# Kernel optimization log

Hardware: AMD Instinct MI355X
Metric: run time of the kernel (lower is better)

The kernel has to match this reference:

```python
import jax, jax.numpy as jnp
import numpy as np

EPS = 1e-5  # torch LayerNorm default

def _layernorm(x, g, b):
    mu = jnp.mean(x, axis=-1, keepdims=True)
    var = jnp.mean(jnp.square(x - mu), axis=-1, keepdims=True)
    return (x - mu) * jax.lax.rsqrt(var + EPS) * g + b

def _gelu(x):
    return jax.nn.gelu(x, approximate=False)  # torch nn.GELU default is exact erf

def setup_inputs() -> dict:
    B, S, D, F = 2, 128, 64, 256
    key = jax.random.key(0)
    ks = jax.random.split(key, 8)
    def xavier(k, fan_in, fan_out, gain=1.0):
        lim = gain * np.sqrt(6.0 / (fan_in + fan_out))
        return jax.random.uniform(k, (fan_in, fan_out), jnp.float32, -lim, lim)
    return {
        "q": jax.random.normal(ks[0], (B, S, D), jnp.float32),
        # gauge generator MLP: Linear(2D, F) -> GELU -> Linear(F, D*D)
        "gw1": xavier(ks[1], 2 * D, F),
        "gb1": jnp.zeros((F,), jnp.float32),
        "gw2": xavier(ks[2], F, D * D, gain=0.01),  # nn.init.xavier_uniform_(gain=0.01)
        "gb2": jnp.zeros((D * D,), jnp.float32),    # nn.init.zeros_
        # block MLP: Linear(D, F) -> GELU -> Linear(F, D)
        "mw1": xavier(ks[3], D, F),
        "mb1": jnp.zeros((F,), jnp.float32),
        "mw2": xavier(ks[4], F, D),
        "mb2": jnp.zeros((D,), jnp.float32),
        # LayerNorms
        "ln1_g": jnp.ones((D,), jnp.float32),
        "ln1_b": jnp.zeros((D,), jnp.float32),
        "ln2_g": jnp.ones((D,), jnp.float32),
        "ln2_b": jnp.zeros((D,), jnp.float32),
    }

def reference(q, gw1, gb1, gw2, gb2, mw1, mb1, mw2, mb2, ln1_g, ln1_b, ln2_g, ln2_b):
    B, S, D = q.shape
    phi = q
    # pairwise features: cat(phi_i, phi_j) -> (B, S, S, 2D)
    phi_i = jnp.broadcast_to(phi[:, :, None, :], (B, S, S, D))
    phi_j = jnp.broadcast_to(phi[:, None, :, :], (B, S, S, D))
    pairs = jnp.concatenate([phi_i, phi_j], axis=-1)
    # gauge MLP -> U_ij in (B, S, S, D, D)
    h = _gelu(pairs @ gw1 + gb1)
    U = (h @ gw2 + gb2).reshape(B, S, S, D, D)
    # aggregate: sum_j U_ij @ phi_j  (contract d with phi feature dim)
    agg = jnp.einsum('bijde,bjd->bie', U, phi)
    # dropout in eval mode = identity
    phi = _layernorm(phi + agg, ln1_g, ln1_b)
    mlp_out = _gelu(phi @ mw1 + mb1) @ mw2 + mb2
    return _layernorm(phi + mlp_out, ln2_g, ln2_b)
```

## Files before the change

kernel.cpp:

```cpp
#include <hip/hip_runtime.h>
#include <math.h>

namespace {

constexpr int NB = 2, NS = 128, ND = 64, NF = 256;

constexpr size_t OFF_W2   = 0;
constexpr size_t SZ_W2    = (size_t)NB * NS * NF * ND;
constexpr size_t OFF_P    = OFF_W2 + SZ_W2;
constexpr size_t SZ_P     = (size_t)NB * NS * NS * ND;
constexpr size_t OFF_AT   = OFF_P + SZ_P;
constexpr size_t SZ_AT    = (size_t)NB * NF * NS;
constexpr size_t OFF_BT   = OFF_AT + SZ_AT;
constexpr size_t SZ_BT    = (size_t)NB * NS * NF;
constexpr size_t OFF_BIAS = OFF_BT + SZ_BT;

__device__ __forceinline__ float gelu_fast(float x) {
  const float xs = fabsf(x) * 0.70710678118654752f;
  const float t = __builtin_amdgcn_rcpf(fmaf(0.3275911f, xs, 1.0f));
  float p = fmaf(1.061405429f, t, -1.453152027f);
  p = fmaf(p, t, 1.421413741f);
  p = fmaf(p, t, -0.284496736f);
  p = fmaf(p, t, 0.254829592f);
  p *= t;
  const float e = __expf(-xs * xs);
  const float erf_ax = fmaf(-p, e, 1.0f);
  const float erf_x = copysignf(erf_ax, x);
  return 0.5f * x * (1.0f + erf_x);
}

constexpr int QT_LD = NS + 4;

__global__ __launch_bounds__(256) void kA_pre(const float* __restrict__ q,
                                              const float* __restrict__ gw1,
                                              const float* __restrict__ gb1,
                                              const float* __restrict__ gw2,
                                              const float* __restrict__ gb2,
                                              float* __restrict__ A_t,
                                              float* __restrict__ Bt,
                                              float* __restrict__ W2,
                                              float* __restrict__ bias_agg) {
  __shared__ __align__(16) float smem[ND * QT_LD + ND * ND];
  const int t = threadIdx.x;
  const int bid = blockIdx.x;
  if (bid < NB * NS) {
    const int b = bid / NS, i = bid % NS;
    float* qrow = smem;
    if (t < ND) qrow[t] = q[((size_t)b * NS + i) * ND + t];
    __syncthreads();
    const int f = t;
    float a = 0.f, bb = gb1[f];
    #pragma unroll 8
    for (int d = 0; d < ND; ++d) {
      const float qd = qrow[d];
      a  += qd * gw1[d * NF + f];
      bb += qd * gw1[(ND + d) * NF + f];
    }
    A_t[((size_t)b * NF + f) * NS + i] = a;
    Bt[((size_t)b * NS + i) * NF + f] = bb;
  } else if (bid < NB * NS + NB * NF) {
    const int idx = bid - NB * NS;
    const int b = idx / NF, f = idx % NF;
    float* qt = smem;
    float* G  = smem + ND * QT_LD;
    for (int r = 0; r < ND * ND / 256; ++r)
      G[t + r * 256] = gw2[(size_t)f * ND * ND + t + r * 256];
    const float* qb = q + (size_t)b * NS * ND;
    for (int r = 0; r < NS * ND / 256; ++r) {
      const int lin = t + r * 256;
      const int j = lin >> 6, d = lin & 63;
      qt[d * QT_LD + j] = qb[lin];
    }
    __syncthreads();
    const int tj = t >> 3, te = t & 7;
    const int j0 = tj * 4, e0 = te * 8;
    float acc[4][8];
    #pragma unroll
    for (int jj = 0; jj < 4; ++jj)
      #pragma unroll
      for (int ee = 0; ee < 8; ++ee) acc[jj][ee] = 0.f;
    #pragma unroll 4
    for (int d = 0; d < ND; ++d) {
      const float4 qv = *(const float4*)&qt[d * QT_LD + j0];
      const float4 g0 = *(const float4*)&G[d * ND + e0];
      const float4 g1 = *(const float4*)&G[d * ND + e0 + 4];
      const float qa[4] = {qv.x, qv.y, qv.z, qv.w};
      const float ga[8] = {g0.x, g0.y, g0.z, g0.w, g1.x, g1.y, g1.z, g1.w};
      #pragma unroll
      for (int jj = 0; jj < 4; ++jj)
        #pragma unroll
        for (int ee = 0; ee < 8; ++ee) acc[jj][ee] += qa[jj] * ga[ee];
    }
    #pragma unroll
    for (int jj = 0; jj < 4; ++jj) {
      const int j = j0 + jj;
      float* dst = W2 + (((size_t)b * NS + j) * NF + f) * ND + e0;
      *(float4*)&dst[0] = make_float4(acc[jj][0], acc[jj][1], acc[jj][2], acc[jj][3]);
      *(float4*)&dst[4] = make_float4(acc[jj][4], acc[jj][5], acc[jj][6], acc[jj][7]);
    }
  } else {
    const int b = bid - (NB * NS + NB * NF);
    float* qs = smem;
    float* colsum = smem + NS * ND;
    const float* qb = q + (size_t)b * NS * ND;
    for (int r = 0; r < NS * ND / 256; ++r) qs[t + r * 256] = qb[t + r * 256];
    __syncthreads();
    if (t < ND) {
      float s = 0.f;
      for (int j = 0; j < NS; ++j) s += qs[j * ND + t];
      colsum[t] = s;
    }
    __syncthreads();
    if (t < ND) {
      float acc = 0.f;
      for (int d = 0; d < ND; ++d) acc += gb2[d * ND + t] * colsum[d];
      bias_agg[b * ND + t] = acc;
    }
  }
}

__global__ __launch_bounds__(512) void k2_main(const float* __restrict__ A_t,
                                               const float* __restrict__ Bt,
                                               const float* __restrict__ W2,
                                               float* __restrict__ P) {
  const int b = blockIdx.x / NS, j = blockIdx.x % NS;
  const int t = threadIdx.x;
  __shared__ float Btj[NF];
  __shared__ __align__(16) float Hc[64 * NS];
  __shared__ __align__(16) float Wc[64 * ND];
  if (t < NF) Btj[t] = Bt[((size_t)b * NS + j) * NF + t];
  const float* W2bj = W2 + ((size_t)b * NS + j) * NF * ND;
  const float* Ab = A_t + (size_t)b * NF * NS;

  const int ty = t >> 4, tx = t & 15;
  const int i0 = ty * 4, e0 = tx * 4;
  const int ih = t & 127, fh = (t >> 7) * 16;
  float acc[4][4];
  #pragma unroll
  for (int r = 0; r < 4; ++r)
    #pragma unroll
    for (int cc = 0; cc < 4; ++cc) acc[r][cc] = 0.f;

  float4 w0 = *(const float4*)&W2bj[t * 8];
  float4 w1 = *(const float4*)&W2bj[t * 8 + 4];

  for (int c = 0; c < NF / 64; ++c) {
    __syncthreads();
    *(float4*)&Wc[t * 8]     = w0;
    *(float4*)&Wc[t * 8 + 4] = w1;
    #pragma unroll 4
    for (int m = 0; m < 16; ++m) {
      const int fc = fh + m;
      const float v = Ab[(c * 64 + fc) * NS + ih] + Btj[c * 64 + fc];
      Hc[fc * NS + ih] = gelu_fast(v);
    }
    if (c < NF / 64 - 1) {
      w0 = *(const float4*)&W2bj[(c + 1) * 64 * ND + t * 8];
      w1 = *(const float4*)&W2bj[(c + 1) * 64 * ND + t * 8 + 4];
    }
    __syncthreads();
    #pragma unroll 4
    for (int fc = 0; fc < 64; ++fc) {
      const float4 h = *(const float4*)&Hc[fc * NS + i0];
      const float4 w = *(const float4*)&Wc[fc * ND + e0];
      const float ha[4] = {h.x, h.y, h.z, h.w};
      const float wa[4] = {w.x, w.y, w.z, w.w};
      #pragma unroll
      for (int r = 0; r < 4; ++r)
        #pragma unroll
        for (int cc = 0; cc < 4; ++cc) acc[r][cc] += ha[r] * wa[cc];
    }
  }
  float* Pbj = P + ((size_t)b * NS + j) * NS * ND;
  #pragma unroll
  for (int r = 0; r < 4; ++r) {
    *(float4*)&Pbj[(size_t)(i0 + r) * ND + e0] =
        make_float4(acc[r][0], acc[r][1], acc[r][2], acc[r][3]);
  }
}

__global__ __launch_bounds__(512) void k3_epi(const float* __restrict__ q,
                                              const float* __restrict__ P,
                                              const float* __restrict__ bias_agg,
                                              const float* __restrict__ mw1,
                                              const float* __restrict__ mb1,
                                              const float* __restrict__ mw2,
                                              const float* __restrict__ mb2,
                                              const float* __restrict__ ln1g,
                                              const float* __restrict__ ln1b,
                                              const float* __restrict__ ln2g,
                                              const float* __restrict__ ln2b,
                                              float* __restrict__ out) {
  const int b = blockIdx.x / NS, i = blockIdx.x % NS;
  const int t = threadIdx.x;
  const int e = t & 63, g = t >> 6;
  __shared__ float red[8 * ND];
  __shared__ float phi1[ND];
  __shared__ float hid[NF];
  const float* Pb = P + (size_t)b * NS * NS * ND;
  float s = 0.f;
  #pragma unroll 4
  for (int m = 0; m < 16; ++m) {
    const int jj = g * 16 + m;
    s += Pb[((size_t)jj * NS + i) * ND + e];
  }
  red[t] = s;
  __syncthreads();
  if (t < ND) {
    float agg = bias_agg[b * ND + e];
    #pragma unroll
    for (int gg = 0; gg < 8; ++gg) agg += red[gg * ND + e];
    const float x = q[((size_t)b * NS + i) * ND + e] + agg;
    float sum = x, sumsq = x * x;
    #pragma unroll
    for (int off = 32; off >= 1; off >>= 1) {
      sum += __shfl_xor(sum, off);
      sumsq += __shfl_xor(sumsq, off);
    }
    const float mu = sum * (1.f / 64.f);
    const float var = sumsq * (1.f / 64.f) - mu * mu;
    const float inv = rsqrtf(var + 1e-5f);
    phi1[e] = (x - mu) * inv * ln1g[e] + ln1b[e];
  }
  __syncthreads();
  if (t < NF) {
    float h = mb1[t];
    #pragma unroll 8
    for (int d = 0; d < ND; ++d) h += phi1[d] * mw1[d * NF + t];
    hid[t] = gelu_fast(h);
  }
  __syncthreads();
  {
    float p = 0.f;
    #pragma unroll 8
    for (int m = 0; m < 32; ++m) {
      const int f = g * 32 + m;
      p += hid[f] * mw2[f * ND + e];
    }
    red[t] = p;
  }
  __syncthreads();
  if (t < ND) {
    float mlp = mb2[e];
    #pragma unroll
    for (int gg = 0; gg < 8; ++gg) mlp += red[gg * ND + e];
    const float x = phi1[e] + mlp;
    float sum = x, sumsq = x * x;
    #pragma unroll
    for (int off = 32; off >= 1; off >>= 1) {
      sum += __shfl_xor(sum, off);
      sumsq += __shfl_xor(sumsq, off);
    }
    const float mu = sum * (1.f / 64.f);
    const float var = sumsq * (1.f / 64.f) - mu * mu;
    const float inv = rsqrtf(var + 1e-5f);
    out[((size_t)b * NS + i) * ND + e] = (x - mu) * inv * ln2g[e] + ln2b[e];
  }
}

}

extern "C" void kernel_launch(void* const* d_in, const int* in_sizes, int n_in,
                              void* d_out, int out_size, void* d_ws, size_t ws_size,
                              hipStream_t stream) {
  const float* q    = (const float*)d_in[0];
  const float* gw1  = (const float*)d_in[1];
  const float* gb1  = (const float*)d_in[2];
  const float* gw2  = (const float*)d_in[3];
  const float* gb2  = (const float*)d_in[4];
  const float* mw1  = (const float*)d_in[5];
  const float* mb1  = (const float*)d_in[6];
  const float* mw2  = (const float*)d_in[7];
  const float* mb2  = (const float*)d_in[8];
  const float* ln1g = (const float*)d_in[9];
  const float* ln1b = (const float*)d_in[10];
  const float* ln2g = (const float*)d_in[11];
  const float* ln2b = (const float*)d_in[12];
  float* out = (float*)d_out;
  float* ws  = (float*)d_ws;

  float* W2   = ws + OFF_W2;
  float* Pp   = ws + OFF_P;
  float* A_t  = ws + OFF_AT;
  float* Bt   = ws + OFF_BT;
  float* bias = ws + OFF_BIAS;

  kA_pre<<<NB * NS + NB * NF + NB, 256, 0, stream>>>(q, gw1, gb1, gw2, gb2,
                                                     A_t, Bt, W2, bias);
  k2_main<<<NB * NS, 512, 0, stream>>>(A_t, Bt, W2, Pp);
  k3_epi<<<NB * NS, 512, 0, stream>>>(q, Pp, bias, mw1, mb1, mw2, mb2,
                                      ln1g, ln1b, ln2g, ln2b, out);
}
```

Before: 124.7 us.

## Use bf16 MFMA for per-pair gauge GEMM in k2_main

Replaces the scalar FP32 outer-product inner loop of k2_main with bf16 MFMA 16x16x32 instructions. The GELU-activated hidden values and the W2 chunk are converted to bf16 and staged in padded LDS tiles. Each wave computes a 32x32 output tile. This targets the FP32 FMA throughput bound of the main GEMM, at the cost of bf16 precision in H and W2. It also drops the software prefetch of W2 and writes the output with scalar stores instead of float4.

```diff
diff --git a/kernel.cpp b/kernel.cpp
--- a/kernel.cpp
+++ b/kernel.cpp
@@ -1,9 +1,14 @@
 #include <hip/hip_runtime.h>
+#include <hip/hip_bf16.h>
 #include <math.h>
 
 namespace {
 
 constexpr int NB = 2, NS = 128, ND = 64, NF = 256;
+
+typedef __attribute__((ext_vector_type(8))) short short8;
+typedef __attribute__((ext_vector_type(8))) unsigned short ushort8;
+typedef __attribute__((ext_vector_type(4))) float floatx4;
 
 constexpr size_t OFF_W2   = 0;
 constexpr size_t SZ_W2    = (size_t)NB * NS * NF * ND;
@@ -119,64 +124,96 @@
   }
 }
 
+constexpr int HLD = 72;
+
 __global__ __launch_bounds__(512) void k2_main(const float* __restrict__ A_t,
                                                const float* __restrict__ Bt,
                                                const float* __restrict__ W2,
                                                float* __restrict__ P) {
   const int b = blockIdx.x / NS, j = blockIdx.x % NS;
   const int t = threadIdx.x;
+  const int lane = t & 63, w = t >> 6;
   __shared__ float Btj[NF];
-  __shared__ __align__(16) float Hc[64 * NS];
-  __shared__ __align__(16) float Wc[64 * ND];
+  __shared__ __align__(16) unsigned short Hc[NS * HLD];
+  __shared__ __align__(16) unsigned short Wc[ND * HLD];
   if (t < NF) Btj[t] = Bt[((size_t)b * NS + j) * NF + t];
+
   const float* W2bj = W2 + ((size_t)b * NS + j) * NF * ND;
   const float* Ab = A_t + (size_t)b * NF * NS;
 
-  const int ty = t >> 4, tx = t & 15;
-  const int i0 = ty * 4, e0 = tx * 4;
-  const int ih = t & 127, fh = (t >> 7) * 16;
-  float acc[4][4];
+  const int wi = (w & 3) * 32, we = (w >> 2) * 32;
+  const int m = lane & 15, quad = lane >> 4;
+
+  const int hi = (w & 1) * 64 + lane;
+  const int hoct0 = t >> 7;
+  const int weid = t & 63, woct = t >> 6;
+
+  floatx4 acc[2][2];
   #pragma unroll
-  for (int r = 0; r < 4; ++r)
-    #pragma unroll
-    for (int cc = 0; cc < 4; ++cc) acc[r][cc] = 0.f;
-
-  float4 w0 = *(const float4*)&W2bj[t * 8];
-  float4 w1 = *(const float4*)&W2bj[t * 8 + 4];
+  for (int a0 = 0; a0 < 2; ++a0)
+    #pragma unroll
+    for (int a1 = 0; a1 < 2; ++a1) acc[a0][a1] = (floatx4)0.f;
 
   for (int c = 0; c < NF / 64; ++c) {
     __syncthreads();
-    *(float4*)&Wc[t * 8]     = w0;
-    *(float4*)&Wc[t * 8 + 4] = w1;
-    #pragma unroll 4
-    for (int m = 0; m < 16; ++m) {
-      const int fc = fh + m;
-      const float v = Ab[(c * 64 + fc) * NS + ih] + Btj[c * 64 + fc];
-      Hc[fc * NS + ih] = gelu_fast(v);
-    }
-    if (c < NF / 64 - 1) {
-      w0 = *(const float4*)&W2bj[(c + 1) * 64 * ND + t * 8];
-      w1 = *(const float4*)&W2bj[(c + 1) * 64 * ND + t * 8 + 4];
-    }
-    __syncthreads();
-    #pragma unroll 4
-    for (int fc = 0; fc < 64; ++fc) {
-      const float4 h = *(const float4*)&Hc[fc * NS + i0];
-      const float4 w = *(const float4*)&Wc[fc * ND + e0];
-      const float ha[4] = {h.x, h.y, h.z, h.w};
-      const float wa[4] = {w.x, w.y, w.z, w.w};
-      #pragma unroll
-      for (int r = 0; r < 4; ++r)
+    float wv[8];
+    #pragma unroll
+    for (int r = 0; r < 8; ++r)
+      wv[r] = W2bj[(size_t)(c * 64 + woct * 8 + r) * ND + weid];
+    float hv[2][8];
+    #pragma unroll
+    for (int s = 0; s < 2; ++s) {
+      const int oct = hoct0 + 4 * s;
+      #pragma unroll
+      for (int r = 0; r < 8; ++r) {
+        const int f = c * 64 + oct * 8 + r;
+        hv[s][r] = gelu_fast(Ab[(size_t)f * NS + hi] + Btj[f]);
+      }
+    }
+    {
+      union { __hip_bfloat162 b2[4]; ushort8 v; } u;
+      #pragma unroll
+      for (int p = 0; p < 4; ++p)
+        u.b2[p] = __float22bfloat162_rn(make_float2(wv[2 * p], wv[2 * p + 1]));
+      *(ushort8*)&Wc[weid * HLD + woct * 8] = u.v;
+    }
+    #pragma unroll
+    for (int s = 0; s < 2; ++s) {
+      union { __hip_bfloat162 b2[4]; ushort8 v; } u;
+      #pragma unroll
+      for (int p = 0; p < 4; ++p)
+        u.b2[p] = __float22bfloat162_rn(make_float2(hv[s][2 * p], hv[s][2 * p + 1]));
+      *(ushort8*)&Hc[hi * HLD + (hoct0 + 4 * s) * 8] = u.v;
+    }
+    __syncthreads();
+    #pragma unroll
+    for (int kk = 0; kk < 2; ++kk) {
+      short8 afr[2], bfr[2];
+      #pragma unroll
+      for (int ti = 0; ti < 2; ++ti)
+        afr[ti] = *(const short8*)&Hc[(wi + ti * 16 + m) * HLD + kk * 32 + quad * 8];
+      #pragma unroll
+      for (int te = 0; te < 2; ++te)
+        bfr[te] = *(const short8*)&Wc[(we + te * 16 + m) * HLD + kk * 32 + quad * 8];
+      #pragma unroll
+      for (int ti = 0; ti < 2; ++ti)
         #pragma unroll
-        for (int cc = 0; cc < 4; ++cc) acc[r][cc] += ha[r] * wa[cc];
+        for (int te = 0; te < 2; ++te)
+          acc[ti][te] = __builtin_amdgcn_mfma_f32_16x16x32_bf16(
+              afr[ti], bfr[te], acc[ti][te], 0, 0, 0);
     }
   }
   float* Pbj = P + ((size_t)b * NS + j) * NS * ND;
   #pragma unroll
-  for (int r = 0; r < 4; ++r) {
-    *(float4*)&Pbj[(size_t)(i0 + r) * ND + e0] =
-        make_float4(acc[r][0], acc[r][1], acc[r][2], acc[r][3]);
-  }
+  for (int ti = 0; ti < 2; ++ti)
+    #pragma unroll
+    for (int te = 0; te < 2; ++te)
+      #pragma unroll
+      for (int r = 0; r < 4; ++r) {
+        const int row = wi + ti * 16 + quad * 4 + r;
+        const int col = we + te * 16 + m;
+        Pbj[(size_t)row * ND + col] = acc[ti][te][r];
+      }
 }
 
 __global__ __launch_bounds__(512) void k3_epi(const float* __restrict__ q,
@@ -200,8 +237,8 @@
   const float* Pb = P + (size_t)b * NS * NS * ND;
   float s = 0.f;
   #pragma unroll 4
-  for (int m = 0; m < 16; ++m) {
-    const int jj = g * 16 + m;
+  for (int m0 = 0; m0 < 16; ++m0) {
+    const int jj = g * 16 + m0;
     s += Pb[((size_t)jj * NS + i) * ND + e];
   }
   red[t] = s;
@@ -233,8 +270,8 @@
   {
     float p = 0.f;
     #pragma unroll 8
-    for (int m = 0; m < 32; ++m) {
-      const int f = g * 32 + m;
+    for (int m0 = 0; m0 < 32; ++m0) {
+      const int f = g * 32 + m0;
       p += hid[f] * mw2[f * ND + e];
     }
     red[t] = p;
```

Measured after the change: 112.9 us. 9.5% less time.
